# Optimization experiments

Hardware: AMD Instinct MI355X
Metric: run time of the kernel (lower is better)

## Reference

```python
import jax, jax.numpy as jnp
import numpy as np

LEAK_RATE = 0.1
SPIKE_THRESHOLD = 0.5
MAX_DIM = 2560
R = 2048   # reservoir dim
D = 1024   # input dim
B = 4096   # batch


def setup_inputs() -> dict:
    key = jax.random.key(0)
    k1, k2, k3, k4, k5 = jax.random.split(key, 5)
    inputs = jax.random.normal(k1, (B, D), dtype=jnp.float32)
    prev_state = jax.random.normal(k2, (B, MAX_DIM), dtype=jnp.float32)
    W_in = jax.random.normal(k3, (R, D), dtype=jnp.float32) * (1.0 / np.sqrt(D))
    W_res = jax.random.normal(k4, (R, R), dtype=jnp.float32) * (1.0 / np.sqrt(R))
    W_gate = jax.random.normal(k5, (3 * R, D), dtype=jnp.float32) * (1.0 / np.sqrt(D))
    return {"inputs": inputs, "prev_state": prev_state,
            "W_in": W_in, "W_res": W_res, "W_gate": W_gate}


def reference(inputs, prev_state, W_in, W_res, W_gate):
    # Slice state to active reservoir width (W_res.shape[0] == R)
    prev = prev_state[:, :R]                                  # [B, R]
    input_part = jnp.matmul(inputs, W_in.T)                   # [B, R]
    reservoir_part = jnp.matmul(prev, W_res.T)                # [B, R]
    gate = jax.nn.sigmoid(jnp.matmul(inputs, W_gate.T))       # [B, 3R]
    i_gate, f_gate, o_gate = jnp.split(gate, 3, axis=-1)      # each [B, R]
    state = (1.0 - LEAK_RATE) * (f_gate * prev) \
        + LEAK_RATE * jnp.tanh(i_gate * (input_part + reservoir_part))
    state = o_gate * state
    # Spike threshold + soft reset
    state = jnp.where(state > SPIKE_THRESHOLD, state - SPIKE_THRESHOLD, state)
    # Pad up to max dynamic reservoir dim
    padded = jnp.pad(state, ((0, 0), (0, MAX_DIM - R)))       # [B, MAX_DIM]
    return padded
```

## Files before the change

### kernel.cpp

```cpp
#include <hip/hip_runtime.h>

#define B_  4096
#define D_  1024
#define R_  2048
#define MAXD 2560

typedef _Float16 half8 __attribute__((ext_vector_type(8)));
typedef _Float16 half4 __attribute__((ext_vector_type(4)));
typedef float    f32x4 __attribute__((ext_vector_type(4)));

constexpr int BM = 128;
constexpr int BN = 64;
constexpr int BK = 32;
constexpr int SAS = 40;

__device__ inline float sigmoidf_(float x) { return 1.0f / (1.0f + expf(-x)); }

__global__ __launch_bounds__(256, 2)
void reservoir_fused(const float* __restrict__ X,
                     const float* __restrict__ P,
                     const float* __restrict__ Win,
                     const float* __restrict__ Wres,
                     const float* __restrict__ Wg,
                     float* __restrict__ out)
{
    __shared__ _Float16 sAh[BM * SAS];
    __shared__ _Float16 sAl[BM * SAS];
    __shared__ _Float16 sWh[4][BN * SAS];
    __shared__ _Float16 sWl[4][BN * SAS];

    const int tid  = threadIdx.x;
    const int lane = tid & 63;
    const int wv   = tid >> 6;
    const int m0   = blockIdx.y * BM;
    const int n0   = blockIdx.x * BN;

    f32x4 acc[4][2][4];
    #pragma unroll
    for (int s = 0; s < 4; ++s)
        #pragma unroll
        for (int mt = 0; mt < 2; ++mt)
            #pragma unroll
            for (int nt = 0; nt < 4; ++nt) acc[s][mt][nt] = (f32x4){0.f, 0.f, 0.f, 0.f};

    const int fr = lane & 15;
    const int fk = (lane >> 4) * 8;

    for (int k0 = 0; k0 < D_ + R_; k0 += BK) {
        const bool ph1 = (k0 < D_);

        {
            const float* src; int ld, kc;
            if (ph1) { src = X; ld = D_;   kc = k0; }
            else     { src = P; ld = MAXD; kc = k0 - D_; }
            #pragma unroll
            for (int i = 0; i < 4; ++i) {
                int f = i * 256 + tid;
                int row = f >> 3, c4 = (f & 7) * 4;
                f32x4 v = *(const f32x4*)(src + (size_t)(m0 + row) * ld + kc + c4);
                half4 h, l;
                #pragma unroll
                for (int j = 0; j < 4; ++j) {
                    h[j] = (_Float16)v[j];
                    l[j] = (_Float16)(v[j] - (float)h[j]);
                }
                *(half4*)(&sAh[row * SAS + c4]) = h;
                *(half4*)(&sAl[row * SAS + c4]) = l;
            }
        }
        {
            const float* src; int ld, kc;
            if (ph1) { src = Win;  ld = D_; kc = k0; }
            else     { src = Wres; ld = R_; kc = k0 - D_; }
            #pragma unroll
            for (int i = 0; i < 2; ++i) {
                int f = i * 256 + tid;
                int row = f >> 3, c4 = (f & 7) * 4;
                f32x4 v = *(const f32x4*)(src + (size_t)(n0 + row) * ld + kc + c4);
                half4 h, l;
                #pragma unroll
                for (int j = 0; j < 4; ++j) {
                    h[j] = (_Float16)v[j];
                    l[j] = (_Float16)(v[j] - (float)h[j]);
                }
                *(half4*)(&sWh[0][row * SAS + c4]) = h;
                *(half4*)(&sWl[0][row * SAS + c4]) = l;
            }
        }
        if (ph1) {
            #pragma unroll
            for (int g = 0; g < 3; ++g)
                #pragma unroll
                for (int i = 0; i < 2; ++i) {
                    int f = i * 256 + tid;
                    int row = f >> 3, c4 = (f & 7) * 4;
                    f32x4 v = *(const f32x4*)(Wg + (size_t)(g * R_ + n0 + row) * D_ + k0 + c4);
                    half4 h, l;
                    #pragma unroll
                    for (int j = 0; j < 4; ++j) {
                        h[j] = (_Float16)v[j];
                        l[j] = (_Float16)(v[j] - (float)h[j]);
                    }
                    *(half4*)(&sWh[1 + g][row * SAS + c4]) = h;
                    *(half4*)(&sWl[1 + g][row * SAS + c4]) = l;
                }
        }
        __syncthreads();

        half8 ah0 = *(const half8*)(&sAh[(wv * 32 +      fr) * SAS + fk]);
        half8 al0 = *(const half8*)(&sAl[(wv * 32 +      fr) * SAS + fk]);
        half8 ah1 = *(const half8*)(&sAh[(wv * 32 + 16 + fr) * SAS + fk]);
        half8 al1 = *(const half8*)(&sAl[(wv * 32 + 16 + fr) * SAS + fk]);

        const int nsets = ph1 ? 4 : 1;
        #pragma unroll
        for (int s = 0; s < 4; ++s) {
            if (s < nsets) {
                #pragma unroll
                for (int nt = 0; nt < 4; ++nt) {
                    half8 bh = *(const half8*)(&sWh[s][(nt * 16 + fr) * SAS + fk]);
                    half8 bl = *(const half8*)(&sWl[s][(nt * 16 + fr) * SAS + fk]);
                    acc[s][0][nt] = __builtin_amdgcn_mfma_f32_16x16x32_f16(ah0, bh, acc[s][0][nt], 0, 0, 0);
                    acc[s][0][nt] = __builtin_amdgcn_mfma_f32_16x16x32_f16(al0, bh, acc[s][0][nt], 0, 0, 0);
                    acc[s][0][nt] = __builtin_amdgcn_mfma_f32_16x16x32_f16(ah0, bl, acc[s][0][nt], 0, 0, 0);
                    acc[s][1][nt] = __builtin_amdgcn_mfma_f32_16x16x32_f16(ah1, bh, acc[s][1][nt], 0, 0, 0);
                    acc[s][1][nt] = __builtin_amdgcn_mfma_f32_16x16x32_f16(al1, bh, acc[s][1][nt], 0, 0, 0);
                    acc[s][1][nt] = __builtin_amdgcn_mfma_f32_16x16x32_f16(ah1, bl, acc[s][1][nt], 0, 0, 0);
                }
            }
        }
        __syncthreads();
    }

    const int qd = lane >> 4;
    #pragma unroll
    for (int mt = 0; mt < 2; ++mt)
        #pragma unroll
        for (int nt = 0; nt < 4; ++nt)
            #pragma unroll
            for (int r = 0; r < 4; ++r) {
                int row = m0 + wv * 32 + mt * 16 + qd * 4 + r;
                int col = n0 + nt * 16 + fr;
                float pre = acc[0][mt][nt][r];
                float ig  = sigmoidf_(acc[1][mt][nt][r]);
                float fg  = sigmoidf_(acc[2][mt][nt][r]);
                float og  = sigmoidf_(acc[3][mt][nt][r]);
                float pv  = P[(size_t)row * MAXD + col];
                float st  = 0.9f * (fg * pv) + 0.1f * tanhf(ig * pre);
                st *= og;
                if (st > 0.5f) st -= 0.5f;
                out[(size_t)row * MAXD + col] = st;
            }
}

__global__ void pad_zero(float* __restrict__ out) {
    int idx = blockIdx.x * 256 + threadIdx.x;
    int row = idx >> 7;
    int c   = (idx & 127) * 4;
    *(f32x4*)(&out[(size_t)row * MAXD + R_ + c]) = (f32x4){0.f, 0.f, 0.f, 0.f};
}

extern "C" void kernel_launch(void* const* d_in, const int* in_sizes, int n_in,
                              void* d_out, int out_size, void* d_ws, size_t ws_size,
                              hipStream_t stream) {
    const float* X    = (const float*)d_in[0];
    const float* P    = (const float*)d_in[1];
    const float* Win  = (const float*)d_in[2];
    const float* Wres = (const float*)d_in[3];
    const float* Wg   = (const float*)d_in[4];
    float* out        = (float*)d_out;

    pad_zero<<<2048, 256, 0, stream>>>(out);
    dim3 grid(R_ / BN, B_ / BM);
    reservoir_fused<<<grid, 256, 0, stream>>>(X, P, Win, Wres, Wg, out);
}
```

Baseline: 509.9 us.

## Prefetch next K-chunk into registers and swizzle LDS layout for MFMA reads

```diff
diff --git a/kernel.cpp b/kernel.cpp
--- a/kernel.cpp
+++ b/kernel.cpp
@@ -12,9 +12,17 @@
 constexpr int BM = 128;
 constexpr int BN = 64;
 constexpr int BK = 32;
-constexpr int SAS = 40;
-
-__device__ inline float sigmoidf_(float x) { return 1.0f / (1.0f + expf(-x)); }
+constexpr int NCHUNK = (D_ + R_) / BK;
+constexpr int NCH1   = D_ / BK;
+
+__device__ __forceinline__ float sigmoidf_(float x) { return 1.0f / (1.0f + expf(-x)); }
+
+__device__ __forceinline__ void wg_barrier() {
+    __builtin_amdgcn_sched_barrier(0);
+    asm volatile("s_waitcnt lgkmcnt(0)" ::: "memory");
+    __builtin_amdgcn_s_barrier();
+    __builtin_amdgcn_sched_barrier(0);
+}
 
 __global__ __launch_bounds__(256, 2)
 void reservoir_fused(const float* __restrict__ X,
@@ -24,10 +32,8 @@
                      const float* __restrict__ Wg,
                      float* __restrict__ out)
 {
-    __shared__ _Float16 sAh[BM * SAS];
-    __shared__ _Float16 sAl[BM * SAS];
-    __shared__ _Float16 sWh[4][BN * SAS];
-    __shared__ _Float16 sWl[4][BN * SAS];
+    __shared__ _Float16 sA[2][8][512];
+    __shared__ _Float16 sW[2][4][4][512];
 
     const int tid  = threadIdx.x;
     const int lane = tid & 63;
@@ -43,95 +49,128 @@
             #pragma unroll
             for (int nt = 0; nt < 4; ++nt) acc[s][mt][nt] = (f32x4){0.f, 0.f, 0.f, 0.f};
 
+    const int crow = tid >> 3;
+    const int c4   = (tid & 7) * 4;
+    const int q    = c4 >> 3;
+    const int fbase = q * 128 + (c4 & 4);
+
+    const int raddr = ((((lane & 15) ^ (lane >> 4)) << 3) + ((lane >> 4) << 7));
+
+    f32x4 pa[4];
+    f32x4 pw[8];
+
+    auto issue_loads = [&](int t) {
+        if (t < NCH1) {
+            const int kc = t * BK + c4;
+            const float* a = X + (size_t)m0 * D_ + kc;
+            #pragma unroll
+            for (int i = 0; i < 4; ++i)
+                pa[i] = *(const f32x4*)(a + (size_t)(crow + 32 * i) * D_);
+            const float* w = Win + (size_t)n0 * D_ + kc;
+            #pragma unroll
+            for (int i = 0; i < 2; ++i)
+                pw[i] = *(const f32x4*)(w + (size_t)(crow + 32 * i) * D_);
+            const float* g = Wg + (size_t)n0 * D_ + kc;
+            #pragma unroll
+            for (int gg = 0; gg < 3; ++gg)
+                #pragma unroll
+                for (int i = 0; i < 2; ++i)
+                    pw[2 + gg * 2 + i] = *(const f32x4*)(g + (size_t)(gg * R_ + crow + 32 * i) * D_);
+        } else {
+            const int kc = t * BK - D_ + c4;
+            const float* a = P + (size_t)m0 * MAXD + kc;
+            #pragma unroll
+            for (int i = 0; i < 4; ++i)
+                pa[i] = *(const f32x4*)(a + (size_t)(crow + 32 * i) * MAXD);
+            const float* w = Wres + (size_t)n0 * R_ + kc;
+            #pragma unroll
+            for (int i = 0; i < 2; ++i)
+                pw[i] = *(const f32x4*)(w + (size_t)(crow + 32 * i) * R_);
+        }
+    };
+
+    auto stage_A = [&]() {
+        #pragma unroll
+        for (int i = 0; i < 4; ++i) {
+            const int r = crow + 32 * i;
+            const int idx = (((r & 15) ^ q) << 3) + fbase;
+            half4 h, l;
+            #pragma unroll
+            for (int j = 0; j < 4; ++j) {
+                float v = pa[i][j];
+                h[j] = (_Float16)v;
+                l[j] = (_Float16)(v - (float)h[j]);
+            }
+            *(half4*)(&sA[0][r >> 4][idx]) = h;
+            *(half4*)(&sA[1][r >> 4][idx]) = l;
+        }
+    };
+    auto stage_W = [&](int nw) {
+        #pragma unroll
+        for (int i = 0; i < 8; ++i) if (i < nw) {
+            const int s   = (i < 2) ? 0 : 1 + ((i - 2) >> 1);
+            const int sub = (i < 2) ? i : ((i - 2) & 1);
+            const int r   = crow + 32 * sub;
+            const int idx = (((r & 15) ^ q) << 3) + fbase;
+            half4 h, l;
+            #pragma unroll
+            for (int j = 0; j < 4; ++j) {
+                float v = pw[i][j];
+                h[j] = (_Float16)v;
+                l[j] = (_Float16)(v - (float)h[j]);
+            }
+            *(half4*)(&sW[0][s][r >> 4][idx]) = h;
+            *(half4*)(&sW[1][s][r >> 4][idx]) = l;
+        }
+    };
+
+#define MFMA_BLOCK(NSETS)                                                                         \
+    {                                                                                             \
+        half8 ah0 = *(const half8*)(&sA[0][wv * 2 + 0][raddr]);                                   \
+        half8 al0 = *(const half8*)(&sA[1][wv * 2 + 0][raddr]);                                   \
+        half8 ah1 = *(const half8*)(&sA[0][wv * 2 + 1][raddr]);                                   \
+        half8 al1 = *(const half8*)(&sA[1][wv * 2 + 1][raddr]);                                   \
+        __builtin_amdgcn_s_setprio(1);                                                            \
+        _Pragma("unroll")                                                                         \
+        for (int s = 0; s < NSETS; ++s) {                                                         \
+            _Pragma("unroll")                                                                     \
+            for (int nt = 0; nt < 4; ++nt) {                                                      \
+                half8 bh = *(const half8*)(&sW[0][s][nt][raddr]);                                 \
+                half8 bl = *(const half8*)(&sW[1][s][nt][raddr]);                                 \
+                acc[s][0][nt] = __builtin_amdgcn_mfma_f32_16x16x32_f16(ah0, bh, acc[s][0][nt], 0, 0, 0); \
+                acc[s][0][nt] = __builtin_amdgcn_mfma_f32_16x16x32_f16(al0, bh, acc[s][0][nt], 0, 0, 0); \
+                acc[s][0][nt] = __builtin_amdgcn_mfma_f32_16x16x32_f16(ah0, bl, acc[s][0][nt], 0, 0, 0); \
+                acc[s][1][nt] = __builtin_amdgcn_mfma_f32_16x16x32_f16(ah1, bh, acc[s][1][nt], 0, 0, 0); \
+                acc[s][1][nt] = __builtin_amdgcn_mfma_f32_16x16x32_f16(al1, bh, acc[s][1][nt], 0, 0, 0); \
+                acc[s][1][nt] = __builtin_amdgcn_mfma_f32_16x16x32_f16(ah1, bl, acc[s][1][nt], 0, 0, 0); \
+            }                                                                                     \
+        }                                                                                         \
+        __builtin_amdgcn_s_setprio(0);                                                            \
+    }
+
+    issue_loads(0);
+
+    #pragma unroll 1
+    for (int t = 0; t < NCH1; ++t) {
+        stage_A();
+        stage_W(8);
+        issue_loads(t + 1);
+        wg_barrier();
+        MFMA_BLOCK(4)
+        wg_barrier();
+    }
+    #pragma unroll 1
+    for (int t = NCH1; t < NCHUNK; ++t) {
+        stage_A();
+        stage_W(2);
+        if (t + 1 < NCHUNK) issue_loads(t + 1);
+        wg_barrier();
+        MFMA_BLOCK(1)
+        wg_barrier();
+    }
+#undef MFMA_BLOCK
+
     const int fr = lane & 15;
-    const int fk = (lane >> 4) * 8;
-
-    for (int k0 = 0; k0 < D_ + R_; k0 += BK) {
-        const bool ph1 = (k0 < D_);
-
-        {
-            const float* src; int ld, kc;
-            if (ph1) { src = X; ld = D_;   kc = k0; }
-            else     { src = P; ld = MAXD; kc = k0 - D_; }
-            #pragma unroll
-            for (int i = 0; i < 4; ++i) {
-                int f = i * 256 + tid;
-                int row = f >> 3, c4 = (f & 7) * 4;
-                f32x4 v = *(const f32x4*)(src + (size_t)(m0 + row) * ld + kc + c4);
-                half4 h, l;
-                #pragma unroll
-                for (int j = 0; j < 4; ++j) {
-                    h[j] = (_Float16)v[j];
-                    l[j] = (_Float16)(v[j] - (float)h[j]);
-                }
-                *(half4*)(&sAh[row * SAS + c4]) = h;
-                *(half4*)(&sAl[row * SAS + c4]) = l;
-            }
-        }
-        {
-            const float* src; int ld, kc;
-            if (ph1) { src = Win;  ld = D_; kc = k0; }
-            else     { src = Wres; ld = R_; kc = k0 - D_; }
-            #pragma unroll
-            for (int i = 0; i < 2; ++i) {
-                int f = i * 256 + tid;
-                int row = f >> 3, c4 = (f & 7) * 4;
-                f32x4 v = *(const f32x4*)(src + (size_t)(n0 + row) * ld + kc + c4);
-                half4 h, l;
-                #pragma unroll
-                for (int j = 0; j < 4; ++j) {
-                    h[j] = (_Float16)v[j];
-                    l[j] = (_Float16)(v[j] - (float)h[j]);
-                }
-                *(half4*)(&sWh[0][row * SAS + c4]) = h;
-                *(half4*)(&sWl[0][row * SAS + c4]) = l;
-            }
-        }
-        if (ph1) {
-            #pragma unroll
-            for (int g = 0; g < 3; ++g)
-                #pragma unroll
-                for (int i = 0; i < 2; ++i) {
-                    int f = i * 256 + tid;
-                    int row = f >> 3, c4 = (f & 7) * 4;
-                    f32x4 v = *(const f32x4*)(Wg + (size_t)(g * R_ + n0 + row) * D_ + k0 + c4);
-                    half4 h, l;
-                    #pragma unroll
-                    for (int j = 0; j < 4; ++j) {
-                        h[j] = (_Float16)v[j];
-                        l[j] = (_Float16)(v[j] - (float)h[j]);
-                    }
-                    *(half4*)(&sWh[1 + g][row * SAS + c4]) = h;
-                    *(half4*)(&sWl[1 + g][row * SAS + c4]) = l;
-                }
-        }
-        __syncthreads();
-
-        half8 ah0 = *(const half8*)(&sAh[(wv * 32 +      fr) * SAS + fk]);
-        half8 al0 = *(const half8*)(&sAl[(wv * 32 +      fr) * SAS + fk]);
-        half8 ah1 = *(const half8*)(&sAh[(wv * 32 + 16 + fr) * SAS + fk]);
-        half8 al1 = *(const half8*)(&sAl[(wv * 32 + 16 + fr) * SAS + fk]);
-
-        const int nsets = ph1 ? 4 : 1;
-        #pragma unroll
-        for (int s = 0; s < 4; ++s) {
-            if (s < nsets) {
-                #pragma unroll
-                for (int nt = 0; nt < 4; ++nt) {
-                    half8 bh = *(const half8*)(&sWh[s][(nt * 16 + fr) * SAS + fk]);
-                    half8 bl = *(const half8*)(&sWl[s][(nt * 16 + fr) * SAS + fk]);
-                    acc[s][0][nt] = __builtin_amdgcn_mfma_f32_16x16x32_f16(ah0, bh, acc[s][0][nt], 0, 0, 0);
-                    acc[s][0][nt] = __builtin_amdgcn_mfma_f32_16x16x32_f16(al0, bh, acc[s][0][nt], 0, 0, 0);
-                    acc[s][0][nt] = __builtin_amdgcn_mfma_f32_16x16x32_f16(ah0, bl, acc[s][0][nt], 0, 0, 0);
-                    acc[s][1][nt] = __builtin_amdgcn_mfma_f32_16x16x32_f16(ah1, bh, acc[s][1][nt], 0, 0, 0);
-                    acc[s][1][nt] = __builtin_amdgcn_mfma_f32_16x16x32_f16(al1, bh, acc[s][1][nt], 0, 0, 0);
-                    acc[s][1][nt] = __builtin_amdgcn_mfma_f32_16x16x32_f16(ah1, bl, acc[s][1][nt], 0, 0, 0);
-                }
-            }
-        }
-        __syncthreads();
-    }
-
     const int qd = lane >> 4;
     #pragma unroll
     for (int mt = 0; mt < 2; ++mt)
```

New measurement: 436.8 us. 1.17x faster.
